# Kernel tuning notes

Measured on AMD Instinct MI355X. Metric: run time of the kernel, lower is better.

## Reference

```python
import jax, jax.numpy as jnp
import numpy as np

B = 8192
IN_CH = 2048
N_SUB = 8
NETWORK_COUNTS = [150, 148, 132, 136, 76, 122, 236]  # 2 * per-hemi counts
OUT_DIM = sum(NETWORK_COUNTS)  # 1000


def setup_inputs() -> dict:
    key = jax.random.key(0)
    k1, k2, k3, k4 = jax.random.split(key, 4)
    scale = 1.0 / (IN_CH ** 0.5)
    x = jax.random.normal(k1, (B, IN_CH), dtype=jnp.float32)
    subject_ids = jax.random.randint(k2, (B,), 0, N_SUB, dtype=jnp.int64)
    # Concatenation of the 7 per-network SubjectLayers weights along the output
    # dim is mathematically identical to running each head and concatenating.
    W = jax.random.normal(k3, (N_SUB, IN_CH, OUT_DIM), dtype=jnp.float32) * scale
    b = jax.random.normal(k4, (N_SUB, OUT_DIM), dtype=jnp.float32) * scale
    return {"x": x, "subject_ids": subject_ids, "W": W, "b": b}


def reference(x, subject_ids, W, b):
    # out[b, o] = sum_d x[b, d] * W[subject_ids[b], d, o] + bias[subject_ids[b], o]
    # Compute scores against all subjects then select, avoiding materializing
    # the (B, IN_CH, OUT_DIM) gathered weight tensor.
    full = jnp.einsum('bd,sdo->bso', x, W)  # (B, N_SUB, OUT_DIM)
    sel = jnp.take_along_axis(full, subject_ids[:, None, None], axis=1)[:, 0, :]
    return sel + b[subject_ids]
```

## Files before the change

kernel.cpp:

```cpp
#include <hip/hip_runtime.h>
#include <hip/hip_bf16.h>
#include <cstdint>
#include <cstddef>

#define NROWS 8192
#define KDIM  2048
#define ODIM  1000
#define NSUB  8
#define OPAD  1024

#define BM 160
#define BN 256
#define BK 64
#define MT_MAX 8
#define ASLOT (BM * BK)
#define SLOT  ((BM + BN) * BK)

typedef __attribute__((ext_vector_type(4))) float f32x4;
typedef __attribute__((ext_vector_type(8))) short short8v;
typedef __attribute__((ext_vector_type(4))) unsigned short u16x4;
typedef __attribute__((ext_vector_type(4))) int int4v;

__device__ __forceinline__ unsigned short f2bf(float f){
  unsigned u = __builtin_bit_cast(unsigned, f);
  unsigned r = (u + 0x7FFFu + ((u >> 16) & 1u)) >> 16;
  return (unsigned short)r;
}

__device__ __forceinline__ void gload16(const void* g, void* l){
  __builtin_amdgcn_global_load_lds(
      (const __attribute__((address_space(1))) void*)g,
      (__attribute__((address_space(3))) void*)l, 16, 0, 0);
}

__global__ __launch_bounds__(256) void build_perm(const int* __restrict__ sid,
                                                  int* __restrict__ counts,
                                                  int* __restrict__ offsets,
                                                  int* __restrict__ perm){
  int s = blockIdx.x;
  __shared__ int shs[NROWS];
  __shared__ int red_lt[4], red_eq[4], wsum[4];
  __shared__ int sh_base;

  int t = threadIdx.x, lane = t & 63, wv = t >> 6;

  int c_lt = 0, c_eq = 0;
  const int4v* sv = (const int4v*)sid;
  #pragma unroll
  for (int i = 0; i < NROWS / 4 / 256; i++){
    int idx = i * 256 + t;
    int4v v = sv[idx];
    *(int4v*)&shs[idx * 4] = v;
    #pragma unroll
    for (int e = 0; e < 4; e++){ c_lt += (v[e] < s); c_eq += (v[e] == s); }
  }
  #pragma unroll
  for (int d = 32; d >= 1; d >>= 1){
    c_lt += __shfl_xor(c_lt, d);
    c_eq += __shfl_xor(c_eq, d);
  }
  if (lane == 0){ red_lt[wv] = c_lt; red_eq[wv] = c_eq; }
  __syncthreads();
  if (t == 0){
    int lt = red_lt[0] + red_lt[1] + red_lt[2] + red_lt[3];
    int eq = red_eq[0] + red_eq[1] + red_eq[2] + red_eq[3];
    offsets[s] = lt;
    counts[s]  = eq;
    sh_base = lt;
  }
  __syncthreads();
  int base = sh_base;

  for (int c0 = 0; c0 < NROWS; c0 += 256){
    int v = shs[c0 + t];
    bool eq = (v == s);
    unsigned long long m = __ballot(eq);
    int rk = __popcll(m & ((1ull << lane) - 1ull));
    int wc = __popcll(m);
    if (lane == 0) wsum[wv] = wc;
    __syncthreads();
    int woff = 0;
    #pragma unroll
    for (int w = 0; w < 4; w++) if (w < wv) woff += wsum[w];
    int tot = wsum[0] + wsum[1] + wsum[2] + wsum[3];
    if (eq) perm[base + woff + rk] = c0 + t;
    base += tot;
    __syncthreads();
  }
}

__global__ __launch_bounds__(256) void cvt_x(const float* __restrict__ x,
                                             unsigned short* __restrict__ xb){
  int b = blockIdx.x;
  int t = threadIdx.x;
  size_t base = (size_t)b * 8192 + (size_t)t * 8;
  #pragma unroll
  for (int c = 0; c < 4; c++){
    size_t f = base + (size_t)c * 2048;
    f32x4 v0 = *(const f32x4*)(x + f);
    f32x4 v1 = *(const f32x4*)(x + f + 4);
    short8v o;
    o[0] = (short)f2bf(v0[0]); o[1] = (short)f2bf(v0[1]);
    o[2] = (short)f2bf(v0[2]); o[3] = (short)f2bf(v0[3]);
    o[4] = (short)f2bf(v1[0]); o[5] = (short)f2bf(v1[1]);
    o[6] = (short)f2bf(v1[2]); o[7] = (short)f2bf(v1[3]);
    *(short8v*)(xb + f) = o;
  }
}

__global__ __launch_bounds__(256) void transpose_w(const float* __restrict__ W,
                                                   unsigned short* __restrict__ Wt){
  __shared__ float tile[64][65];
  int b = blockIdx.x;
  int t = threadIdx.x;
  int s  = b >> 9;
  int kt = (b >> 4) & 31;
  int ot = b & 15;
  int k0 = kt * 64, o0 = ot * 64;

  int kr  = t >> 4;
  int ol4 = (t & 15) * 4;
  bool lval = (o0 + ol4) < ODIM;

  const float* src = W + ((size_t)s * KDIM + k0) * ODIM + o0;
  #pragma unroll
  for (int it = 0; it < 4; it++){
    int k = kr + it * 16;
    f32x4 v = lval ? *(const f32x4*)(src + (size_t)k * ODIM + ol4)
                   : f32x4{0.f, 0.f, 0.f, 0.f};
    tile[k][ol4 + 0] = v[0]; tile[k][ol4 + 1] = v[1];
    tile[k][ol4 + 2] = v[2]; tile[k][ol4 + 3] = v[3];
  }
  __syncthreads();

  int j8   = (t & 7) * 8;
  int orow = t >> 3;
  unsigned short* dst = Wt + ((size_t)(s * OPAD + o0)) * KDIM + k0;
  #pragma unroll
  for (int it = 0; it < 2; it++){
    int o = orow + it * 32;
    bool oval = (o0 + o) < ODIM;
    short8v w;
    #pragma unroll
    for (int j = 0; j < 8; j++)
      w[j] = oval ? (short)f2bf(tile[j8 + j][o]) : (short)0;
    *(short8v*)(dst + (size_t)o * KDIM + j8) = w;
  }
}

__global__ __launch_bounds__(512, 1) void gemm_bf16(
    const unsigned short* __restrict__ xb,
    const unsigned short* __restrict__ Wt,
    const int* __restrict__ counts,
    const int* __restrict__ offsets,
    const int* __restrict__ perm,
    const float* __restrict__ bias,
    float* __restrict__ out)
{
  int b  = blockIdx.x;
  int s  = b & 7;
  int r  = b >> 3;
  int nt = r & 3;
  int mt = r >> 2;
  int cnt = counts[s];
  int loc0 = mt * BM;
  if (loc0 >= cnt) return;
  int row0 = offsets[s] + loc0;
  int cnt_loc = cnt - loc0;

  __shared__ unsigned short L[3 * SLOT];
  __shared__ int permL[BM];

  int t = threadIdx.x;
  int lane = t & 63;
  int wave = t >> 6;

  int wm = (wave >> 2) * 80;
  int wn = (wave & 3) << 6;
  int frow = lane & 15, fk = lane >> 4;
  int axor = frow & 7;

  int srck = (((lane & 7) ^ ((lane >> 3) & 7)) << 3);

  int prow[5];
  if (wave < 4){
    #pragma unroll
    for (int i = 0; i < 5; i++){
      int row = ((wave * 5 + i) << 3) + (lane >> 3);
      int pidx = row0 + row; if (pidx > NROWS - 1) pidx = NROWS - 1;
      prow[i] = perm[pidx];
    }
  }
  {
    int pr = t;
    if (pr >= 320) pr -= 320;
    if (pr >= 160) pr -= 160;
    int pidx = row0 + pr; if (pidx > NROWS - 1) pidx = NROWS - 1;
    int pl = perm[pidx];
    asm volatile("s_waitcnt vmcnt(0)" ::: "memory");
    __builtin_amdgcn_sched_barrier(0);
    permL[pr] = pl;
  }

  size_t gA[5]; unsigned loA[5];
  size_t gB[6]; unsigned loB[6];
  if (wave < 4){
    #pragma unroll
    for (int i = 0; i < 5; i++){
      int ca = wave * 5 + i;
      gA[i]  = (size_t)prow[i] * KDIM + srck;
      loA[i] = (unsigned)((ca << 9) + (lane << 3));
    }
    #pragma unroll
    for (int j = 0; j < 2; j++){
      int cb  = wave * 2 + j;
      int row = (cb << 3) + (lane >> 3);
      gB[j]  = ((size_t)(s * OPAD + nt * BN + row)) * KDIM + srck;
      loB[j] = (unsigned)(ASLOT + (cb << 9) + (lane << 3));
    }
  } else {
    #pragma unroll
    for (int j = 0; j < 6; j++){
      int cb  = 8 + (wave - 4) * 6 + j;
      int row = (cb << 3) + (lane >> 3);
      gB[j]  = ((size_t)(s * OPAD + nt * BN + row)) * KDIM + srck;
      loB[j] = (unsigned)(ASLOT + (cb << 9) + (lane << 3));
    }
  }

  f32x4 acc[5][4];
  #pragma unroll
  for (int i = 0; i < 5; i++)
    #pragma unroll
    for (int j = 0; j < 4; j++)
      #pragma unroll
      for (int e = 0; e < 4; e++) acc[i][j][e] = 0.f;

#define STAGE_FULL(sl, koff) do { \
    unsigned short* Ls = &L[(sl) * SLOT]; \
    if (wave < 4){ \
      gload16(xb + gA[0] + (koff), (void*)(Ls + loA[0])); \
      gload16(xb + gA[1] + (koff), (void*)(Ls + loA[1])); \
      gload16(xb + gA[2] + (koff), (void*)(Ls + loA[2])); \
      gload16(xb + gA[3] + (koff), (void*)(Ls + loA[3])); \
      gload16(xb + gA[4] + (koff), (void*)(Ls + loA[4])); \
      gload16(Wt + gB[0] + (koff), (void*)(Ls + loB[0])); \
      gload16(Wt + gB[1] + (koff), (void*)(Ls + loB[1])); \
    } else { \
      gload16(Wt + gB[0] + (koff), (void*)(Ls + loB[0])); \
      gload16(Wt + gB[1] + (koff), (void*)(Ls + loB[1])); \
      gload16(Wt + gB[2] + (koff), (void*)(Ls + loB[2])); \
      gload16(Wt + gB[3] + (koff), (void*)(Ls + loB[3])); \
      gload16(Wt + gB[4] + (koff), (void*)(Ls + loB[4])); \
      gload16(Wt + gB[5] + (koff), (void*)(Ls + loB[5])); \
    } \
  } while (0)

#define STAGE_P0(sl, koff) do { \
    unsigned short* Ls = &L[(sl) * SLOT]; \
    if (wave < 4){ \
      gload16(xb + gA[0] + (koff), (void*)(Ls + loA[0])); \
      gload16(xb + gA[1] + (koff), (void*)(Ls + loA[1])); \
      gload16(xb + gA[2] + (koff), (void*)(Ls + loA[2])); \
      gload16(xb + gA[3] + (koff), (void*)(Ls + loA[3])); \
      gload16(xb + gA[4] + (koff), (void*)(Ls + loA[4])); \
    } else { \
      gload16(Wt + gB[0] + (koff), (void*)(Ls + loB[0])); \
      gload16(Wt + gB[1] + (koff), (void*)(Ls + loB[1])); \
      gload16(Wt + gB[2] + (koff), (void*)(Ls + loB[2])); \
    } \
  } while (0)
#define STAGE_P1(sl, koff) do { \
    unsigned short* Ls = &L[(sl) * SLOT]; \
    if (wave < 4){ \
      gload16(Wt + gB[0] + (koff), (void*)(Ls + loB[0])); \
      gload16(Wt + gB[1] + (koff), (void*)(Ls + loB[1])); \
    } else { \
      gload16(Wt + gB[3] + (koff), (void*)(Ls + loB[3])); \
      gload16(Wt + gB[4] + (koff), (void*)(Ls + loB[4])); \
      gload16(Wt + gB[5] + (koff), (void*)(Ls + loB[5])); \
    } \
  } while (0)

#define VMN() do { \
    if (wave < 4) asm volatile("s_waitcnt vmcnt(7)" ::: "memory"); \
    else          asm volatile("s_waitcnt vmcnt(6)" ::: "memory"); \
    __builtin_amdgcn_sched_barrier(0); \
  } while (0)
#define VM0() do { \
    asm volatile("s_waitcnt vmcnt(0)" ::: "memory"); \
    __builtin_amdgcn_sched_barrier(0); \
  } while (0)

#define AOFF(mi, ks) (((wm + ((mi) << 4) + frow) << 6) + ((((ks) * 4 + fk) ^ axor) << 3))
#define BOFF(ni, ks) (ASLOT + ((wn + ((ni) << 4) + frow) << 6) + ((((ks) * 4 + fk) ^ axor) << 3))
#define MF(mi, ni, av, bv) acc[mi][ni] = __builtin_amdgcn_mfma_f32_16x16x32_bf16(av, bv, acc[mi][ni], 0, 0, 0)

#define PH(sl, ks, STG, ENDW) do { \
    const unsigned short* Lb = &L[(sl) * SLOT]; \
    short8v a0 = *(const short8v*)&Lb[AOFF(0, ks)]; \
    short8v a1 = *(const short8v*)&Lb[AOFF(1, ks)]; \
    short8v a2 = *(const short8v*)&Lb[AOFF(2, ks)]; \
    short8v a3 = *(const short8v*)&Lb[AOFF(3, ks)]; \
    short8v a4 = *(const short8v*)&Lb[AOFF(4, ks)]; \
    short8v b0 = *(const short8v*)&Lb[BOFF(0, ks)]; \
    short8v b1 = *(const short8v*)&Lb[BOFF(1, ks)]; \
    short8v b2 = *(const short8v*)&Lb[BOFF(2, ks)]; \
    short8v b3 = *(const short8v*)&Lb[BOFF(3, ks)]; \
    STG; \
    __builtin_amdgcn_s_barrier(); \
    asm volatile("s_waitcnt lgkmcnt(0)" ::: "memory"); \
    __builtin_amdgcn_sched_barrier(0); \
    __builtin_amdgcn_s_setprio(1); \
    MF(0, 0, a0, b0); MF(1, 0, a1, b0); MF(2, 0, a2, b0); MF(3, 0, a3, b0); MF(4, 0, a4, b0); \
    MF(0, 1, a0, b1); MF(1, 1, a1, b1); MF(2, 1, a2, b1); MF(3, 1, a3, b1); MF(4, 1, a4, b1); \
    MF(0, 2, a0, b2); MF(1, 2, a1, b2); MF(2, 2, a2, b2); MF(3, 2, a3, b2); MF(4, 2, a4, b2); \
    MF(0, 3, a0, b3); MF(1, 3, a1, b3); MF(2, 3, a2, b3); MF(3, 3, a3, b3); MF(4, 3, a4, b3); \
    __builtin_amdgcn_s_setprio(0); \
    ENDW; \
    __builtin_amdgcn_s_barrier(); \
  } while (0)

  STAGE_FULL(0, 0);
  STAGE_FULL(1, BK);
  VMN();
  __builtin_amdgcn_s_barrier();

  for (int i = 0; i < 10; ++i){
    int kb = i * 3 * BK;
    PH(0, 0, STAGE_P0(2, kb + 2 * BK), );
    PH(0, 1, STAGE_P1(2, kb + 2 * BK), VMN());
    PH(1, 0, STAGE_P0(0, kb + 3 * BK), );
    PH(1, 1, STAGE_P1(0, kb + 3 * BK), VMN());
    PH(2, 0, STAGE_P0(1, kb + 4 * BK), );
    PH(2, 1, STAGE_P1(1, kb + 4 * BK), VMN());
  }
  PH(0, 0, , );
  PH(0, 1, , VM0());
  PH(1, 0, , );
  PH(1, 1, , );

  float bvn[4]; int ocol[4];
  #pragma unroll
  for (int ni = 0; ni < 4; ni++){
    int o = nt * BN + wn + (ni << 4) + frow;
    ocol[ni] = o;
    bvn[ni] = (o < ODIM) ? bias[s * ODIM + o] : 0.f;
  }
  #pragma unroll
  for (int mi = 0; mi < 5; mi++){
    int rbase = wm + (mi << 4) + (fk << 2);
    #pragma unroll
    for (int jj = 0; jj < 4; jj++){
      int rr = rbase + jj;
      if (rr < cnt_loc){
        int orow = permL[rr];
        #pragma unroll
        for (int ni = 0; ni < 4; ni++){
          if (ocol[ni] < ODIM)
            out[(size_t)orow * ODIM + ocol[ni]] = acc[mi][ni][jj] + bvn[ni];
        }
      }
    }
  }
#undef STAGE_FULL
#undef STAGE_P0
#undef STAGE_P1
#undef VMN
#undef VM0
#undef AOFF
#undef BOFF
#undef MF
#undef PH
}

__global__ __launch_bounds__(256) void naive_kernel(const float* __restrict__ x,
                                                    const int* __restrict__ sid,
                                                    const float* __restrict__ W,
                                                    const float* __restrict__ bias,
                                                    float* __restrict__ out){
  __shared__ float xr[KDIM];
  int row = blockIdx.x;
  int s = sid[row];
  for (int i = threadIdx.x; i < KDIM; i += 256) xr[i] = x[(size_t)row * KDIM + i];
  __syncthreads();
  int o = blockIdx.y * 256 + threadIdx.x;
  if (o >= ODIM) return;
  const float* w = W + (size_t)s * KDIM * ODIM + o;
  float acc = bias[s * ODIM + o];
  for (int k = 0; k < KDIM; k++) acc = fmaf(xr[k], w[(size_t)k * ODIM], acc);
  out[(size_t)row * ODIM + o] = acc;
}

extern "C" void kernel_launch(void* const* d_in, const int* in_sizes, int n_in,
                              void* d_out, int out_size, void* d_ws, size_t ws_size,
                              hipStream_t stream) {
  const float* x    = (const float*)d_in[0];
  const int*   sid  = (const int*)d_in[1];
  const float* W    = (const float*)d_in[2];
  const float* bias = (const float*)d_in[3];
  float* out = (float*)d_out;

  const size_t XB_BYTES = (size_t)NROWS * KDIM * 2;
  const size_t WT_BYTES = (size_t)NSUB * OPAD * KDIM * 2;
  const size_t need = 64 + (size_t)NROWS * 4 + XB_BYTES + WT_BYTES;

  if (ws_size < need){
    naive_kernel<<<dim3(NROWS, 4), 256, 0, stream>>>(x, sid, W, bias, out);
    return;
  }

  char* w = (char*)d_ws;
  int* counts  = (int*)w;
  int* offsets = counts + 8;
  int* perm    = (int*)(w + 64);
  unsigned short* xb = (unsigned short*)(w + 64 + (size_t)NROWS * 4);
  unsigned short* Wt = xb + (size_t)NROWS * KDIM;

  build_perm  <<<NSUB, 256, 0, stream>>>(sid, counts, offsets, perm);
  cvt_x       <<<2048, 256, 0, stream>>>(x, xb);
  transpose_w <<<4096, 256, 0, stream>>>(W, Wt);
  gemm_bf16   <<<NSUB * 4 * MT_MAX, 512, 0, stream>>>(xb, Wt, counts, offsets, perm, bias, out);
}
```

Measured before the change: 100.1 us.

## Split K across two blocks with atomic accumulation and larger M tile

The grouped GEMM now splits the K dimension in two, so twice as many blocks each cover half of K. The M tile grows from 160 to 256 rows and the K step shrinks from 64 to 32. Partial sums are combined with float atomicAdd into an output zeroed by a memset, and only the first K half adds the bias. The aim is better CU occupancy and operand reuse, at the cost of an extra memset pass, atomic write traffic, and a summation order that is no longer deterministic.

```diff
diff --git a/kernel.cpp b/kernel.cpp
--- a/kernel.cpp
+++ b/kernel.cpp
@@ -9,10 +9,13 @@
 #define NSUB  8
 #define OPAD  1024
 
-#define BM 160
+#define BM 256
 #define BN 256
-#define BK 64
-#define MT_MAX 8
+#define BK 32
+#define KSPLIT 2
+#define KHALF (KDIM / KSPLIT)
+#define NT 4
+#define MT_MAX 5
 #define ASLOT (BM * BK)
 #define SLOT  ((BM + BN) * BK)
 
@@ -161,12 +164,15 @@
   int s  = b & 7;
   int r  = b >> 3;
   int nt = r & 3;
-  int mt = r >> 2;
+  int r2 = r >> 2;
+  int mt = r2 % MT_MAX;
+  int kh = r2 / MT_MAX;
   int cnt = counts[s];
   int loc0 = mt * BM;
   if (loc0 >= cnt) return;
   int row0 = offsets[s] + loc0;
   int cnt_loc = cnt - loc0;
+  size_t kbase = (size_t)kh * KHALF;
 
   __shared__ unsigned short L[3 * SLOT];
   __shared__ int permL[BM];
@@ -175,26 +181,22 @@
   int lane = t & 63;
   int wave = t >> 6;
 
-  int wm = (wave >> 2) * 80;
+  int wm = (wave >> 2) << 7;
   int wn = (wave & 3) << 6;
   int frow = lane & 15, fk = lane >> 4;
-  int axor = frow & 7;
-
-  int srck = (((lane & 7) ^ ((lane >> 3) & 7)) << 3);
-
-  int prow[5];
-  if (wave < 4){
-    #pragma unroll
-    for (int i = 0; i < 5; i++){
-      int row = ((wave * 5 + i) << 3) + (lane >> 3);
-      int pidx = row0 + row; if (pidx > NROWS - 1) pidx = NROWS - 1;
-      prow[i] = perm[pidx];
-    }
+  int axor2 = (frow >> 1) & 3;
+
+  int srck = (((lane & 3) ^ ((lane >> 3) & 3)) << 3);
+
+  int prow[2];
+  #pragma unroll
+  for (int rr = 0; rr < 2; rr++){
+    int row = rr * 128 + wave * 16 + (lane >> 2);
+    int pidx = row0 + row; if (pidx > NROWS - 1) pidx = NROWS - 1;
+    prow[rr] = perm[pidx];
   }
   {
-    int pr = t;
-    if (pr >= 320) pr -= 320;
-    if (pr >= 160) pr -= 160;
+    int pr = t & 255;
     int pidx = row0 + pr; if (pidx > NROWS - 1) pidx = NROWS - 1;
     int pl = perm[pidx];
     asm volatile("s_waitcnt vmcnt(0)" ::: "memory");
@@ -202,89 +204,37 @@
     permL[pr] = pl;
   }
 
-  size_t gA[5]; unsigned loA[5];
-  size_t gB[6]; unsigned loB[6];
-  if (wave < 4){
-    #pragma unroll
-    for (int i = 0; i < 5; i++){
-      int ca = wave * 5 + i;
-      gA[i]  = (size_t)prow[i] * KDIM + srck;
-      loA[i] = (unsigned)((ca << 9) + (lane << 3));
-    }
-    #pragma unroll
-    for (int j = 0; j < 2; j++){
-      int cb  = wave * 2 + j;
-      int row = (cb << 3) + (lane >> 3);
-      gB[j]  = ((size_t)(s * OPAD + nt * BN + row)) * KDIM + srck;
-      loB[j] = (unsigned)(ASLOT + (cb << 9) + (lane << 3));
-    }
-  } else {
-    #pragma unroll
-    for (int j = 0; j < 6; j++){
-      int cb  = 8 + (wave - 4) * 6 + j;
-      int row = (cb << 3) + (lane >> 3);
-      gB[j]  = ((size_t)(s * OPAD + nt * BN + row)) * KDIM + srck;
-      loB[j] = (unsigned)(ASLOT + (cb << 9) + (lane << 3));
-    }
-  }
-
-  f32x4 acc[5][4];
-  #pragma unroll
-  for (int i = 0; i < 5; i++)
+  size_t gA[2], gB[2]; unsigned loA[2], loB[2];
+  #pragma unroll
+  for (int rr = 0; rr < 2; rr++){
+    int row = rr * 128 + wave * 16 + (lane >> 2);
+    gA[rr] = (size_t)prow[rr] * KDIM + kbase + srck;
+    gB[rr] = ((size_t)(s * OPAD + nt * BN + row)) * KDIM + kbase + srck;
+    loA[rr] = (unsigned)(row * BK + (lane & 3) * 8);
+    loB[rr] = (unsigned)(ASLOT + row * BK + (lane & 3) * 8);
+  }
+
+  f32x4 acc[8][4];
+  #pragma unroll
+  for (int i = 0; i < 8; i++)
     #pragma unroll
     for (int j = 0; j < 4; j++)
       #pragma unroll
       for (int e = 0; e < 4; e++) acc[i][j][e] = 0.f;
 
-#define STAGE_FULL(sl, koff) do { \
+#define STAGE_A(sl, koff) do { \
     unsigned short* Ls = &L[(sl) * SLOT]; \
-    if (wave < 4){ \
-      gload16(xb + gA[0] + (koff), (void*)(Ls + loA[0])); \
-      gload16(xb + gA[1] + (koff), (void*)(Ls + loA[1])); \
-      gload16(xb + gA[2] + (koff), (void*)(Ls + loA[2])); \
-      gload16(xb + gA[3] + (koff), (void*)(Ls + loA[3])); \
-      gload16(xb + gA[4] + (koff), (void*)(Ls + loA[4])); \
-      gload16(Wt + gB[0] + (koff), (void*)(Ls + loB[0])); \
-      gload16(Wt + gB[1] + (koff), (void*)(Ls + loB[1])); \
-    } else { \
-      gload16(Wt + gB[0] + (koff), (void*)(Ls + loB[0])); \
-      gload16(Wt + gB[1] + (koff), (void*)(Ls + loB[1])); \
-      gload16(Wt + gB[2] + (koff), (void*)(Ls + loB[2])); \
-      gload16(Wt + gB[3] + (koff), (void*)(Ls + loB[3])); \
-      gload16(Wt + gB[4] + (koff), (void*)(Ls + loB[4])); \
-      gload16(Wt + gB[5] + (koff), (void*)(Ls + loB[5])); \
-    } \
-  } while (0)
-
-#define STAGE_P0(sl, koff) do { \
+    gload16(xb + gA[0] + (koff), (void*)(Ls + loA[0])); \
+    gload16(xb + gA[1] + (koff), (void*)(Ls + loA[1])); \
+  } while (0)
+#define STAGE_B(sl, koff) do { \
     unsigned short* Ls = &L[(sl) * SLOT]; \
-    if (wave < 4){ \
-      gload16(xb + gA[0] + (koff), (void*)(Ls + loA[0])); \
-      gload16(xb + gA[1] + (koff), (void*)(Ls + loA[1])); \
-      gload16(xb + gA[2] + (koff), (void*)(Ls + loA[2])); \
-      gload16(xb + gA[3] + (koff), (void*)(Ls + loA[3])); \
-      gload16(xb + gA[4] + (koff), (void*)(Ls + loA[4])); \
-    } else { \
-      gload16(Wt + gB[0] + (koff), (void*)(Ls + loB[0])); \
-      gload16(Wt + gB[1] + (koff), (void*)(Ls + loB[1])); \
-      gload16(Wt + gB[2] + (koff), (void*)(Ls + loB[2])); \
-    } \
-  } while (0)
-#define STAGE_P1(sl, koff) do { \
-    unsigned short* Ls = &L[(sl) * SLOT]; \
-    if (wave < 4){ \
-      gload16(Wt + gB[0] + (koff), (void*)(Ls + loB[0])); \
-      gload16(Wt + gB[1] + (koff), (void*)(Ls + loB[1])); \
-    } else { \
-      gload16(Wt + gB[3] + (koff), (void*)(Ls + loB[3])); \
-      gload16(Wt + gB[4] + (koff), (void*)(Ls + loB[4])); \
-      gload16(Wt + gB[5] + (koff), (void*)(Ls + loB[5])); \
-    } \
+    gload16(Wt + gB[0] + (koff), (void*)(Ls + loB[0])); \
+    gload16(Wt + gB[1] + (koff), (void*)(Ls + loB[1])); \
   } while (0)
 
 #define VMN() do { \
-    if (wave < 4) asm volatile("s_waitcnt vmcnt(7)" ::: "memory"); \
-    else          asm volatile("s_waitcnt vmcnt(6)" ::: "memory"); \
+    asm volatile("s_waitcnt vmcnt(4)" ::: "memory"); \
     __builtin_amdgcn_sched_barrier(0); \
   } while (0)
 #define VM0() do { \
@@ -292,63 +242,72 @@
     __builtin_amdgcn_sched_barrier(0); \
   } while (0)
 
-#define AOFF(mi, ks) (((wm + ((mi) << 4) + frow) << 6) + ((((ks) * 4 + fk) ^ axor) << 3))
-#define BOFF(ni, ks) (ASLOT + ((wn + ((ni) << 4) + frow) << 6) + ((((ks) * 4 + fk) ^ axor) << 3))
+#define AOFF(mi) (((wm + ((mi) << 4) + frow) * BK) + ((fk ^ axor2) << 3))
+#define BOFF(ni) (ASLOT + ((wn + ((ni) << 4) + frow) * BK) + ((fk ^ axor2) << 3))
 #define MF(mi, ni, av, bv) acc[mi][ni] = __builtin_amdgcn_mfma_f32_16x16x32_bf16(av, bv, acc[mi][ni], 0, 0, 0)
 
-#define PH(sl, ks, STG, ENDW) do { \
+#define TILE(sl, SA, SB, ENDW) do { \
     const unsigned short* Lb = &L[(sl) * SLOT]; \
-    short8v a0 = *(const short8v*)&Lb[AOFF(0, ks)]; \
-    short8v a1 = *(const short8v*)&Lb[AOFF(1, ks)]; \
-    short8v a2 = *(const short8v*)&Lb[AOFF(2, ks)]; \
-    short8v a3 = *(const short8v*)&Lb[AOFF(3, ks)]; \
-    short8v a4 = *(const short8v*)&Lb[AOFF(4, ks)]; \
-    short8v b0 = *(const short8v*)&Lb[BOFF(0, ks)]; \
-    short8v b1 = *(const short8v*)&Lb[BOFF(1, ks)]; \
-    short8v b2 = *(const short8v*)&Lb[BOFF(2, ks)]; \
-    short8v b3 = *(const short8v*)&Lb[BOFF(3, ks)]; \
-    STG; \
+    short8v a0 = *(const short8v*)&Lb[AOFF(0)]; \
+    short8v a1 = *(const short8v*)&Lb[AOFF(1)]; \
+    short8v a2 = *(const short8v*)&Lb[AOFF(2)]; \
+    short8v a3 = *(const short8v*)&Lb[AOFF(3)]; \
+    short8v b0 = *(const short8v*)&Lb[BOFF(0)]; \
+    short8v b1 = *(const short8v*)&Lb[BOFF(1)]; \
+    short8v b2 = *(const short8v*)&Lb[BOFF(2)]; \
+    short8v b3 = *(const short8v*)&Lb[BOFF(3)]; \
+    SA; \
     __builtin_amdgcn_s_barrier(); \
     asm volatile("s_waitcnt lgkmcnt(0)" ::: "memory"); \
     __builtin_amdgcn_sched_barrier(0); \
     __builtin_amdgcn_s_setprio(1); \
-    MF(0, 0, a0, b0); MF(1, 0, a1, b0); MF(2, 0, a2, b0); MF(3, 0, a3, b0); MF(4, 0, a4, b0); \
-    MF(0, 1, a0, b1); MF(1, 1, a1, b1); MF(2, 1, a2, b1); MF(3, 1, a3, b1); MF(4, 1, a4, b1); \
-    MF(0, 2, a0, b2); MF(1, 2, a1, b2); MF(2, 2, a2, b2); MF(3, 2, a3, b2); MF(4, 2, a4, b2); \
-    MF(0, 3, a0, b3); MF(1, 3, a1, b3); MF(2, 3, a2, b3); MF(3, 3, a3, b3); MF(4, 3, a4, b3); \
+    MF(0, 0, a0, b0); MF(1, 0, a1, b0); MF(2, 0, a2, b0); MF(3, 0, a3, b0); \
+    MF(0, 1, a0, b1); MF(1, 1, a1, b1); MF(2, 1, a2, b1); MF(3, 1, a3, b1); \
+    MF(0, 2, a0, b2); MF(1, 2, a1, b2); MF(2, 2, a2, b2); MF(3, 2, a3, b2); \
+    MF(0, 3, a0, b3); MF(1, 3, a1, b3); MF(2, 3, a2, b3); MF(3, 3, a3, b3); \
+    __builtin_amdgcn_s_setprio(0); \
+    __builtin_amdgcn_s_barrier(); \
+    short8v a4 = *(const short8v*)&Lb[AOFF(4)]; \
+    short8v a5 = *(const short8v*)&Lb[AOFF(5)]; \
+    short8v a6 = *(const short8v*)&Lb[AOFF(6)]; \
+    short8v a7 = *(const short8v*)&Lb[AOFF(7)]; \
+    SB; \
+    __builtin_amdgcn_s_barrier(); \
+    asm volatile("s_waitcnt lgkmcnt(0)" ::: "memory"); \
+    __builtin_amdgcn_sched_barrier(0); \
+    __builtin_amdgcn_s_setprio(1); \
+    MF(4, 0, a4, b0); MF(5, 0, a5, b0); MF(6, 0, a6, b0); MF(7, 0, a7, b0); \
+    MF(4, 1, a4, b1); MF(5, 1, a5, b1); MF(6, 1, a6, b1); MF(7, 1, a7, b1); \
+    MF(4, 2, a4, b2); MF(5, 2, a5, b2); MF(6, 2, a6, b2); MF(7, 2, a7, b2); \
+    MF(4, 3, a4, b3); MF(5, 3, a5, b3); MF(6, 3, a6, b3); MF(7, 3, a7, b3); \
     __builtin_amdgcn_s_setprio(0); \
     ENDW; \
     __builtin_amdgcn_s_barrier(); \
   } while (0)
 
-  STAGE_FULL(0, 0);
-  STAGE_FULL(1, BK);
+  STAGE_A(0, 0); STAGE_B(0, 0);
+  STAGE_A(1, BK); STAGE_B(1, BK);
   VMN();
   __builtin_amdgcn_s_barrier();
 
   for (int i = 0; i < 10; ++i){
     int kb = i * 3 * BK;
-    PH(0, 0, STAGE_P0(2, kb + 2 * BK), );
-    PH(0, 1, STAGE_P1(2, kb + 2 * BK), VMN());
-    PH(1, 0, STAGE_P0(0, kb + 3 * BK), );
-    PH(1, 1, STAGE_P1(0, kb + 3 * BK), VMN());
-    PH(2, 0, STAGE_P0(1, kb + 4 * BK), );
-    PH(2, 1, STAGE_P1(1, kb + 4 * BK), VMN());
-  }
-  PH(0, 0, , );
-  PH(0, 1, , VM0());
-  PH(1, 0, , );
-  PH(1, 1, , );
+    TILE(0, STAGE_A(2, kb + 2 * BK), STAGE_B(2, kb + 2 * BK), VMN());
+    TILE(1, STAGE_A(0, kb + 3 * BK), STAGE_B(0, kb + 3 * BK), VMN());
+    TILE(2, STAGE_A(1, kb + 4 * BK), STAGE_B(1, kb + 4 * BK), VMN());
+  }
+  TILE(0, , , VM0());
+  TILE(1, , , );
 
   float bvn[4]; int ocol[4];
   #pragma unroll
   for (int ni = 0; ni < 4; ni++){
     int o = nt * BN + wn + (ni << 4) + frow;
     ocol[ni] = o;
-    bvn[ni] = (o < ODIM) ? bias[s * ODIM + o] : 0.f;
-  }
-  #pragma unroll
-  for (int mi = 0; mi < 5; mi++){
+    bvn[ni] = (kh == 0 && o < ODIM) ? bias[s * ODIM + o] : 0.f;
+  }
+  #pragma unroll
+  for (int mi = 0; mi < 8; mi++){
     int rbase = wm + (mi << 4) + (fk << 2);
     #pragma unroll
     for (int jj = 0; jj < 4; jj++){
@@ -358,20 +317,19 @@
         #pragma unroll
         for (int ni = 0; ni < 4; ni++){
           if (ocol[ni] < ODIM)
-            out[(size_t)orow * ODIM + ocol[ni]] = acc[mi][ni][jj] + bvn[ni];
+            atomicAdd(&out[(size_t)orow * ODIM + ocol[ni]], acc[mi][ni][jj] + bvn[ni]);
         }
       }
     }
   }
-#undef STAGE_FULL
-#undef STAGE_P0
-#undef STAGE_P1
+#undef STAGE_A
+#undef STAGE_B
 #undef VMN
 #undef VM0
 #undef AOFF
 #undef BOFF
 #undef MF
-#undef PH
+#undef TILE
 }
 
 __global__ __launch_bounds__(256) void naive_kernel(const float* __restrict__ x,
@@ -417,8 +375,10 @@
   unsigned short* xb = (unsigned short*)(w + 64 + (size_t)NROWS * 4);
   unsigned short* Wt = xb + (size_t)NROWS * KDIM;
 
+  hipMemsetAsync(out, 0, (size_t)NROWS * ODIM * sizeof(float), stream);
+
   build_perm  <<<NSUB, 256, 0, stream>>>(sid, counts, offsets, perm);
   cvt_x       <<<2048, 256, 0, stream>>>(x, xb);
   transpose_w <<<4096, 256, 0, stream>>>(W, Wt);
-  gemm_bf16   <<<NSUB * 4 * MT_MAX, 512, 0, stream>>>(xb, Wt, counts, offsets, perm, bias, out);
-}
+  gemm_bf16   <<<NSUB * NT * MT_MAX * KSPLIT, 512, 0, stream>>>(xb, Wt, counts, offsets, perm, bias, out);
+}
```

Result: slower. 188.1 us (+88.0%).

## Cut GEMM barriers to one per K-tile and fuse perm build with x conversion

Applied to the files above, without the earlier changes.

The GEMM main loop had two workgroup barriers in each half-tile phase, four per K-tile. It now has a single barrier at the end of each full tile, after the wait for outstanding loads. This relies on the three-slot LDS ring to keep staging writes from overlapping slots still being read, and it lets waves drift further apart within a tile. Separately, the permutation build and the fp32-to-bf16 conversion of x now run as one launch, removing a kernel launch. The cost there is that the conversion blocks also reserve the 32 KB of static shared memory used by the permutation blocks.

```diff
diff --git a/kernel.cpp b/kernel.cpp
--- a/kernel.cpp
+++ b/kernel.cpp
@@ -33,17 +33,38 @@
       (__attribute__((address_space(3))) void*)l, 16, 0, 0);
 }
 
-__global__ __launch_bounds__(256) void build_perm(const int* __restrict__ sid,
-                                                  int* __restrict__ counts,
-                                                  int* __restrict__ offsets,
-                                                  int* __restrict__ perm){
-  int s = blockIdx.x;
+__global__ __launch_bounds__(256) void perm_cvt(const int* __restrict__ sid,
+                                                int* __restrict__ counts,
+                                                int* __restrict__ offsets,
+                                                int* __restrict__ perm,
+                                                const float* __restrict__ x,
+                                                unsigned short* __restrict__ xb){
+  int b = blockIdx.x;
+  int t = threadIdx.x;
+
+  if (b >= 8){
+    size_t base = (size_t)(b - 8) * 8192 + (size_t)t * 8;
+    #pragma unroll
+    for (int c = 0; c < 4; c++){
+      size_t f = base + (size_t)c * 2048;
+      f32x4 v0 = *(const f32x4*)(x + f);
+      f32x4 v1 = *(const f32x4*)(x + f + 4);
+      short8v o;
+      o[0] = (short)f2bf(v0[0]); o[1] = (short)f2bf(v0[1]);
+      o[2] = (short)f2bf(v0[2]); o[3] = (short)f2bf(v0[3]);
+      o[4] = (short)f2bf(v1[0]); o[5] = (short)f2bf(v1[1]);
+      o[6] = (short)f2bf(v1[2]); o[7] = (short)f2bf(v1[3]);
+      *(short8v*)(xb + f) = o;
+    }
+    return;
+  }
+
+  int s = b;
   __shared__ int shs[NROWS];
   __shared__ int red_lt[4], red_eq[4], wsum[4];
   __shared__ int sh_base;
 
-  int t = threadIdx.x, lane = t & 63, wv = t >> 6;
-
+  int lane = t & 63, wv = t >> 6;
   int c_lt = 0, c_eq = 0;
   const int4v* sv = (const int4v*)sid;
   #pragma unroll
@@ -86,25 +107,6 @@
     if (eq) perm[base + woff + rk] = c0 + t;
     base += tot;
     __syncthreads();
-  }
-}
-
-__global__ __launch_bounds__(256) void cvt_x(const float* __restrict__ x,
-                                             unsigned short* __restrict__ xb){
-  int b = blockIdx.x;
-  int t = threadIdx.x;
-  size_t base = (size_t)b * 8192 + (size_t)t * 8;
-  #pragma unroll
-  for (int c = 0; c < 4; c++){
-    size_t f = base + (size_t)c * 2048;
-    f32x4 v0 = *(const f32x4*)(x + f);
-    f32x4 v1 = *(const f32x4*)(x + f + 4);
-    short8v o;
-    o[0] = (short)f2bf(v0[0]); o[1] = (short)f2bf(v0[1]);
-    o[2] = (short)f2bf(v0[2]); o[3] = (short)f2bf(v0[3]);
-    o[4] = (short)f2bf(v1[0]); o[5] = (short)f2bf(v1[1]);
-    o[6] = (short)f2bf(v1[2]); o[7] = (short)f2bf(v1[3]);
-    *(short8v*)(xb + f) = o;
   }
 }
 
@@ -296,7 +298,7 @@
 #define BOFF(ni, ks) (ASLOT + ((wn + ((ni) << 4) + frow) << 6) + ((((ks) * 4 + fk) ^ axor) << 3))
 #define MF(mi, ni, av, bv) acc[mi][ni] = __builtin_amdgcn_mfma_f32_16x16x32_bf16(av, bv, acc[mi][ni], 0, 0, 0)
 
-#define PH(sl, ks, STG, ENDW) do { \
+#define PH(sl, ks, STG) do { \
     const unsigned short* Lb = &L[(sl) * SLOT]; \
     short8v a0 = *(const short8v*)&Lb[AOFF(0, ks)]; \
     short8v a1 = *(const short8v*)&Lb[AOFF(1, ks)]; \
@@ -308,7 +310,6 @@
     short8v b2 = *(const short8v*)&Lb[BOFF(2, ks)]; \
     short8v b3 = *(const short8v*)&Lb[BOFF(3, ks)]; \
     STG; \
-    __builtin_amdgcn_s_barrier(); \
     asm volatile("s_waitcnt lgkmcnt(0)" ::: "memory"); \
     __builtin_amdgcn_sched_barrier(0); \
     __builtin_amdgcn_s_setprio(1); \
@@ -317,6 +318,11 @@
     MF(0, 2, a0, b2); MF(1, 2, a1, b2); MF(2, 2, a2, b2); MF(3, 2, a3, b2); MF(4, 2, a4, b2); \
     MF(0, 3, a0, b3); MF(1, 3, a1, b3); MF(2, 3, a2, b3); MF(3, 3, a3, b3); MF(4, 3, a4, b3); \
     __builtin_amdgcn_s_setprio(0); \
+  } while (0)
+
+#define TILE(sl, S0, S1, ENDW) do { \
+    PH(sl, 0, S0); \
+    PH(sl, 1, S1); \
     ENDW; \
     __builtin_amdgcn_s_barrier(); \
   } while (0)
@@ -328,17 +334,13 @@
 
   for (int i = 0; i < 10; ++i){
     int kb = i * 3 * BK;
-    PH(0, 0, STAGE_P0(2, kb + 2 * BK), );
-    PH(0, 1, STAGE_P1(2, kb + 2 * BK), VMN());
-    PH(1, 0, STAGE_P0(0, kb + 3 * BK), );
-    PH(1, 1, STAGE_P1(0, kb + 3 * BK), VMN());
-    PH(2, 0, STAGE_P0(1, kb + 4 * BK), );
-    PH(2, 1, STAGE_P1(1, kb + 4 * BK), VMN());
-  }
-  PH(0, 0, , );
-  PH(0, 1, , VM0());
-  PH(1, 0, , );
-  PH(1, 1, , );
+    TILE(0, STAGE_P0(2, kb + 2 * BK), STAGE_P1(2, kb + 2 * BK), VMN());
+    TILE(1, STAGE_P0(0, kb + 3 * BK), STAGE_P1(0, kb + 3 * BK), VMN());
+    TILE(2, STAGE_P0(1, kb + 4 * BK), STAGE_P1(1, kb + 4 * BK), VMN());
+  }
+  TILE(0, , , VM0());
+  PH(1, 0, );
+  PH(1, 1, );
 
   float bvn[4]; int ocol[4];
   #pragma unroll
@@ -372,6 +374,7 @@
 #undef BOFF
 #undef MF
 #undef PH
+#undef TILE
 }
 
 __global__ __launch_bounds__(256) void naive_kernel(const float* __restrict__ x,
@@ -417,8 +420,7 @@
   unsigned short* xb = (unsigned short*)(w + 64 + (size_t)NROWS * 4);
   unsigned short* Wt = xb + (size_t)NROWS * KDIM;
 
-  build_perm  <<<NSUB, 256, 0, stream>>>(sid, counts, offsets, perm);
-  cvt_x       <<<2048, 256, 0, stream>>>(x, xb);
+  perm_cvt    <<<8 + 2048, 256, 0, stream>>>(sid, counts, offsets, perm, x, xb);
   transpose_w <<<4096, 256, 0, stream>>>(W, Wt);
   gemm_bf16   <<<NSUB * 4 * MT_MAX, 512, 0, stream>>>(xb, Wt, counts, offsets, perm, bias, out);
 }
```

Result: faster. 87.39 us (-12.7%).
